# Kernel tuning notes

Measured on AMD Instinct MI355X. Metric: run time of the kernel, lower is better.

Reference implementation:

```python
import jax, jax.numpy as jnp
import numpy as np

NUM_HEADS = 16
HEAD_DIM = 64
WINDOW = 128        # local attention radius |i-j| <= WINDOW
GLOBAL_STRIDE = 64  # tokens at multiples of GLOBAL_STRIDE attend/are attended globally
NEG_INF = -1e9


def sparse_mask(seq_len):
    # bool [S, S]: local band plus global rows/cols (Longformer-style pattern)
    i = jnp.arange(seq_len)
    local = jnp.abs(i[:, None] - i[None, :]) <= WINDOW
    is_global = (i % GLOBAL_STRIDE) == 0
    return local | is_global[:, None] | is_global[None, :]


def setup_inputs() -> dict:
    key = jax.random.key(0)
    k1, k2, k3 = jax.random.split(key, 3)
    B, S, H = 1, 2048, 1024
    x = jax.random.normal(k1, (B, S, H), dtype=jnp.float32)
    Wqkv = jax.random.normal(k2, (3 * H, H), dtype=jnp.float32) * (1.0 / np.sqrt(H))
    Wout = jax.random.normal(k3, (H, H), dtype=jnp.float32) * (1.0 / np.sqrt(H))
    return {"x": x, "Wqkv": Wqkv, "Wout": Wout}


def reference(x, Wqkv, Wout):
    B, S, H = x.shape
    hd = HEAD_DIM
    scale = 1.0 / np.sqrt(hd)

    qkv = x @ Wqkv.T                       # [B, S, 3H] (torch Linear: x @ W^T)
    q, k, v = jnp.split(qkv, 3, axis=-1)
    # [B, nH, S, hd]
    q = q.reshape(B, S, NUM_HEADS, hd).transpose(0, 2, 1, 3)
    k = k.reshape(B, S, NUM_HEADS, hd).transpose(0, 2, 1, 3)
    v = v.reshape(B, S, NUM_HEADS, hd).transpose(0, 2, 1, 3)

    mask = sparse_mask(S)                  # [S, S] bool, broadcasts over (B, nH)
    scores = jnp.einsum('bhqd,bhkd->bhqk', q, k) * scale
    scores = jnp.where(mask, scores, NEG_INF)
    attn = jax.nn.softmax(scores, axis=-1)  # every row has valid keys -> no NaN
    out = jnp.einsum('bhqk,bhkd->bhqd', attn, v)
    out = out.transpose(0, 2, 1, 3).reshape(B, S, H)
    return out @ Wout.T
```

## Files before the change

kernel.cpp:

```cpp
#include <hip/hip_runtime.h>
#include <hip/hip_bf16.h>
#include <math.h>

#define SEQ   2048
#define HID   1024
#define NH    16
#define HD    64
#define WIN   128
#define GSTR  64

typedef __attribute__((ext_vector_type(8))) short short8;
typedef __attribute__((ext_vector_type(4))) float f32x4;
typedef unsigned short ushort_t;

__device__ inline unsigned short bf16b(float f) {
    union { float f; unsigned int u; } v; v.f = f;
    return (unsigned short)((v.u + 0x7FFFu + ((v.u >> 16) & 1u)) >> 16);
}
__device__ inline float blo(unsigned int u) {
    union { unsigned int i; float f; } v; v.i = u << 16; return v.f;
}
__device__ inline float bhi(unsigned int u) {
    union { unsigned int i; float f; } v; v.i = u & 0xFFFF0000u; return v.f;
}

#define GLOAD_LDS16(gp, lp)                                                    \
    __builtin_amdgcn_global_load_lds(                                          \
        (const __attribute__((address_space(1))) unsigned int*)(gp),           \
        (__attribute__((address_space(3))) unsigned int*)(lp), 16, 0, 0)

__global__ __launch_bounds__(256) void cvt_bf16(const float4* __restrict__ x,
                                                const float4* __restrict__ wq,
                                                const float4* __restrict__ wo,
                                                ushort4* __restrict__ x16,
                                                ushort4* __restrict__ wq16,
                                                ushort4* __restrict__ wo16) {
    for (int idx = blockIdx.x * 256 + threadIdx.x; idx < 1572864;
         idx += gridDim.x * 256) {
        const float4* src; ushort4* dst; int off;
        if (idx < 524288)       { src = x;  dst = x16;  off = idx; }
        else if (idx < 1310720) { src = wq; dst = wq16; off = idx - 524288; }
        else                    { src = wo; dst = wo16; off = idx - 1310720; }
        float4 v = src[off];
        ushort4 o;
        o.x = bf16b(v.x); o.y = bf16b(v.y); o.z = bf16b(v.z); o.w = bf16b(v.w);
        dst[off] = o;
    }
}

template <int BM, int BN, typename OT>
__global__ __launch_bounds__(256) void gemm_bt16(const unsigned short* __restrict__ A,
                                                 const unsigned short* __restrict__ B,
                                                 OT* __restrict__ C,
                                                 int M, int N, int K) {
    constexpr int MI = BM / 32;
    constexpr int NJ = BN / 32;
    __shared__ unsigned short As[BM * 32];
    __shared__ unsigned short Bs[BN * 32];

    const int tid  = threadIdx.x;
    const int wave = tid >> 6;
    const int lane = tid & 63;
    const int quad = lane >> 4;
    const int l15  = lane & 15;
    const int bm = blockIdx.y * BM;
    const int bn = blockIdx.x * BN;
    const int wm = (wave & 1) * (BM / 2);
    const int wn = (wave >> 1) * (BN / 2);
    const int srow = lane >> 2;
    const int scol = (lane & 3) * 8;

    f32x4 acc[MI][NJ];
    #pragma unroll
    for (int i = 0; i < MI; ++i)
        #pragma unroll
        for (int j = 0; j < NJ; ++j)
            acc[i][j] = (f32x4){0.f, 0.f, 0.f, 0.f};

    for (int k0 = 0; k0 < K; k0 += 32) {
        #pragma unroll
        for (int t = 0; t < BM / 64; ++t) {
            const int row = wave * (BM / 4) + t * 16 + srow;
            GLOAD_LDS16(A + (size_t)(bm + row) * K + k0 + scol,
                        &As[(size_t)row * 32 + scol]);
        }
        #pragma unroll
        for (int t = 0; t < BN / 64; ++t) {
            const int row = wave * (BN / 4) + t * 16 + srow;
            GLOAD_LDS16(B + (size_t)(bn + row) * K + k0 + scol,
                        &Bs[(size_t)row * 32 + scol]);
        }
        __syncthreads();

        short8 a[MI], b[NJ];
        #pragma unroll
        for (int im = 0; im < MI; ++im)
            a[im] = *(const short8*)&As[(wm + im * 16 + l15) * 32 + quad * 8];
        #pragma unroll
        for (int jn = 0; jn < NJ; ++jn)
            b[jn] = *(const short8*)&Bs[(wn + jn * 16 + l15) * 32 + quad * 8];

        #pragma unroll
        for (int im = 0; im < MI; ++im)
            #pragma unroll
            for (int jn = 0; jn < NJ; ++jn)
                acc[im][jn] = __builtin_amdgcn_mfma_f32_16x16x32_bf16(
                    a[im], b[jn], acc[im][jn], 0, 0, 0);
        __syncthreads();
    }

    #pragma unroll
    for (int im = 0; im < MI; ++im)
        #pragma unroll
        for (int jn = 0; jn < NJ; ++jn)
            #pragma unroll
            for (int reg = 0; reg < 4; ++reg) {
                const int r = bm + wm + im * 16 + quad * 4 + reg;
                const int c = bn + wn + jn * 16 + l15;
                float v = acc[im][jn][reg];
                if constexpr (sizeof(OT) == 2)
                    C[(size_t)r * N + c] = (OT)bf16b(v);
                else
                    C[(size_t)r * N + c] = (OT)v;
            }
}

__global__ __launch_bounds__(256) void attn_fused(const unsigned short* __restrict__ qkv16,
                                                  unsigned short* __restrict__ aout16) {
    __shared__ __align__(16) unsigned char smem[38912];
    const int tid = threadIdx.x;
    const int h = blockIdx.y;
    const int w    = tid >> 6;
    const int lane = tid & 63;
    const int quad = lane >> 4;
    const int l15  = lane & 15;

    if (blockIdx.x < 32) {
        ushort_t* Qs = (ushort_t*)smem;
        ushort_t* Ks = (ushort_t*)(smem + 9216);
        ushort_t* Vt = (ushort_t*)(smem + 18432);
        ushort_t* Ps = (ushort_t*)(smem + 27648);

        const int bq = blockIdx.x;
        const int q0 = bq * 64;
        const int qi = q0 + w * 16 + l15;

        for (int f = tid; f < 512; f += 256) {
            int row = f >> 3, c8 = f & 7;
            *(uint4*)&Qs[row * 72 + c8 * 8] =
                *(const uint4*)&qkv16[(size_t)(q0 + row) * (3 * HID) + h * HD + c8 * 8];
        }

        float mq = -1.0e30f, lq = 0.f;
        f32x4 Oacc[4];
        #pragma unroll
        for (int jt = 0; jt < 4; ++jt) Oacc[jt] = (f32x4){0.f, 0.f, 0.f, 0.f};

        const int t0 = max(bq - 2, 0);
        const int t1 = min(bq + 2, SEQ / 64 - 1);

        uint4 pk[2];
        uint2 pva[2], pvb[2];

        auto prefetch = [&](int tt2, bool g2) {
            const int nf = g2 ? 256 : 512;
            #pragma unroll
            for (int u = 0; u < 2; ++u) {
                const int f = tid + u * 256;
                if (f < nf) {
                    const int row = f >> 3, c8 = f & 7;
                    const size_t gb = (size_t)(g2 ? (row << 6) : (tt2 * 64 + row))
                                          * (3 * HID) + HID + h * HD + c8 * 8;
                    pk[u] = *(const uint4*)&qkv16[gb];
                    const int kp = f >> 4, dc = f & 15;
                    const int k0i = 2 * kp, k1i = 2 * kp + 1;
                    const size_t b0 = (size_t)(g2 ? (k0i << 6) : (tt2 * 64 + k0i))
                                          * (3 * HID) + 2 * HID + h * HD + dc * 4;
                    const size_t b1 = (size_t)(g2 ? (k1i << 6) : (tt2 * 64 + k1i))
                                          * (3 * HID) + 2 * HID + h * HD + dc * 4;
                    pva[u] = *(const uint2*)&qkv16[b0];
                    pvb[u] = *(const uint2*)&qkv16[b1];
                }
            }
        };
        auto commit = [&](bool g2) {
            const int nf = g2 ? 256 : 512;
            #pragma unroll
            for (int u = 0; u < 2; ++u) {
                const int f = tid + u * 256;
                if (f < nf) {
                    const int row = f >> 3, c8 = f & 7;
                    *(uint4*)&Ks[row * 72 + c8 * 8] = pk[u];
                    const int kp = f >> 4, dc = f & 15;
                    uint2 va = pva[u], vb = pvb[u];
                    unsigned int w0 = (va.x & 0xFFFFu) | (vb.x << 16);
                    unsigned int w1 = (va.x >> 16)     | (vb.x & 0xFFFF0000u);
                    unsigned int w2 = (va.y & 0xFFFFu) | (vb.y << 16);
                    unsigned int w3 = (va.y >> 16)     | (vb.y & 0xFFFF0000u);
                    *(unsigned int*)&Vt[(dc * 4 + 0) * 72 + 2 * kp] = w0;
                    *(unsigned int*)&Vt[(dc * 4 + 1) * 72 + 2 * kp] = w1;
                    *(unsigned int*)&Vt[(dc * 4 + 2) * 72 + 2 * kp] = w2;
                    *(unsigned int*)&Vt[(dc * 4 + 3) * 72 + 2 * kp] = w3;
                }
            }
        };

        prefetch(t0, false);
        commit(false);
        __syncthreads();

        for (int tt = t0; tt <= t1 + 1; ++tt) {
            const bool gather = (tt == t1 + 1);
            const bool hasnext = (tt < t1 + 1);
            if (hasnext) prefetch(tt + 1, (tt + 1) == t1 + 1);

            short8 bQ0 = *(const short8*)&Qs[(w * 16 + l15) * 72 + quad * 8];
            short8 bQ1 = *(const short8*)&Qs[(w * 16 + l15) * 72 + 32 + quad * 8];
            f32x4 st[4];
            #pragma unroll
            for (int kt = 0; kt < 4; ++kt) {
                short8 aK0 = *(const short8*)&Ks[(kt * 16 + l15) * 72 + quad * 8];
                short8 aK1 = *(const short8*)&Ks[(kt * 16 + l15) * 72 + 32 + quad * 8];
                f32x4 z = (f32x4){0.f, 0.f, 0.f, 0.f};
                z = __builtin_amdgcn_mfma_f32_16x16x32_bf16(aK0, bQ0, z, 0, 0, 0);
                z = __builtin_amdgcn_mfma_f32_16x16x32_bf16(aK1, bQ1, z, 0, 0, 0);
                st[kt] = z;
            }

            float sv[4][4];
            float tm = -1.0e30f;
            #pragma unroll
            for (int kt = 0; kt < 4; ++kt)
                #pragma unroll
                for (int reg = 0; reg < 4; ++reg) {
                    const int c = kt * 16 + quad * 4 + reg;
                    const int j = gather ? (c << 6) : (tt * 64 + c);
                    const bool valid = gather ? ((c < 32) && (abs(qi - j) > WIN))
                                              : (abs(qi - j) <= WIN);
                    sv[kt][reg] = valid ? st[kt][reg] * 0.125f : -1.0e30f;
                    tm = fmaxf(tm, sv[kt][reg]);
                }

            tm = fmaxf(tm, __shfl_xor(tm, 16));
            tm = fmaxf(tm, __shfl_xor(tm, 32));
            const float mn = fmaxf(mq, tm);
            const float alpha = __expf(mq - mn);
            float p[4][4];
            float ts = 0.f;
            #pragma unroll
            for (int kt = 0; kt < 4; ++kt)
                #pragma unroll
                for (int reg = 0; reg < 4; ++reg) {
                    p[kt][reg] = __expf(sv[kt][reg] - mn);
                    ts += p[kt][reg];
                }
            ts += __shfl_xor(ts, 16);
            ts += __shfl_xor(ts, 32);
            lq = lq * alpha + ts;
            mq = mn;

            #pragma unroll
            for (int kt = 0; kt < 4; ++kt) {
                ushort4 pkt;
                pkt.x = bf16b(p[kt][0]); pkt.y = bf16b(p[kt][1]);
                pkt.z = bf16b(p[kt][2]); pkt.w = bf16b(p[kt][3]);
                *(ushort4*)&Ps[(w * 16 + l15) * 72 + kt * 16 + quad * 4] = pkt;
            }
            #pragma unroll
            for (int jt = 0; jt < 4; ++jt) {
                Oacc[jt][0] *= alpha; Oacc[jt][1] *= alpha;
                Oacc[jt][2] *= alpha; Oacc[jt][3] *= alpha;
            }

            short8 bP0 = *(const short8*)&Ps[(w * 16 + l15) * 72 + quad * 8];
            short8 bP1 = *(const short8*)&Ps[(w * 16 + l15) * 72 + 32 + quad * 8];
            #pragma unroll
            for (int jt = 0; jt < 4; ++jt) {
                short8 aV0 = *(const short8*)&Vt[(jt * 16 + l15) * 72 + quad * 8];
                short8 aV1 = *(const short8*)&Vt[(jt * 16 + l15) * 72 + 32 + quad * 8];
                Oacc[jt] = __builtin_amdgcn_mfma_f32_16x16x32_bf16(aV0, bP0, Oacc[jt], 0, 0, 0);
                Oacc[jt] = __builtin_amdgcn_mfma_f32_16x16x32_bf16(aV1, bP1, Oacc[jt], 0, 0, 0);
            }

            if (hasnext) {
                __syncthreads();
                commit((tt + 1) == t1 + 1);
                __syncthreads();
            }
        }

        if (!(w == 0 && l15 == 0)) {
            const float inv = 1.0f / lq;
            #pragma unroll
            for (int jt = 0; jt < 4; ++jt) {
                ushort4 o;
                o.x = bf16b(Oacc[jt][0] * inv);
                o.y = bf16b(Oacc[jt][1] * inv);
                o.z = bf16b(Oacc[jt][2] * inv);
                o.w = bf16b(Oacc[jt][3] * inv);
                *(ushort4*)&aout16[(size_t)qi * HID + h * HD + jt * 16 + quad * 4] = o;
            }
        }
    } else {
        const int gh = blockIdx.x - 32;
        ushort_t* Ksw = (ushort_t*)(smem + w * 9728);
        ushort_t* Vtw = (ushort_t*)(smem + w * 9728 + 4608);
        ushort_t* Psw = (ushort_t*)(smem + w * 9728 + 8704);

        const size_t qrow = (size_t)((gh * 16 + l15) * 64) * (3 * HID) + h * HD;
        short8 bQ0 = *(const short8*)&qkv16[qrow + quad * 8];
        short8 bQ1 = *(const short8*)&qkv16[qrow + 32 + quad * 8];

        float mq = -1.0e30f, lq = 0.f;
        f32x4 Oacc[4];
        #pragma unroll
        for (int jt = 0; jt < 4; ++jt) Oacc[jt] = (f32x4){0.f, 0.f, 0.f, 0.f};

        for (int s = 0; s < 16; ++s) {
            const int kb = w * 512 + s * 32;
            #pragma unroll
            for (int u = 0; u < 4; ++u) {
                const int unit = lane + u * 64;
                const int row = unit >> 3, c8 = unit & 7;
                *(uint4*)&Ksw[row * 72 + c8 * 8] =
                    *(const uint4*)&qkv16[(size_t)(kb + row) * (3 * HID) + HID + h * HD + c8 * 8];
            }
            #pragma unroll
            for (int u = 0; u < 4; ++u) {
                const int unit = lane + u * 64;
                const int kp = unit >> 4, dc = unit & 15;
                const size_t b0 = (size_t)(kb + 2 * kp) * (3 * HID) + 2 * HID + h * HD + dc * 4;
                const size_t b1 = b0 + 3 * HID;
                uint2 va = *(const uint2*)&qkv16[b0];
                uint2 vb = *(const uint2*)&qkv16[b1];
                unsigned int w0 = (va.x & 0xFFFFu) | (vb.x << 16);
                unsigned int w1 = (va.x >> 16)     | (vb.x & 0xFFFF0000u);
                unsigned int w2 = (va.y & 0xFFFFu) | (vb.y << 16);
                unsigned int w3 = (va.y >> 16)     | (vb.y & 0xFFFF0000u);
                *(unsigned int*)&Vtw[(dc * 4 + 0) * 32 + 2 * kp] = w0;
                *(unsigned int*)&Vtw[(dc * 4 + 1) * 32 + 2 * kp] = w1;
                *(unsigned int*)&Vtw[(dc * 4 + 2) * 32 + 2 * kp] = w2;
                *(unsigned int*)&Vtw[(dc * 4 + 3) * 32 + 2 * kp] = w3;
            }

            f32x4 st[2];
            #pragma unroll
            for (int kt = 0; kt < 2; ++kt) {
                short8 aK0 = *(const short8*)&Ksw[(kt * 16 + l15) * 72 + quad * 8];
                short8 aK1 = *(const short8*)&Ksw[(kt * 16 + l15) * 72 + 32 + quad * 8];
                f32x4 z = (f32x4){0.f, 0.f, 0.f, 0.f};
                z = __builtin_amdgcn_mfma_f32_16x16x32_bf16(aK0, bQ0, z, 0, 0, 0);
                z = __builtin_amdgcn_mfma_f32_16x16x32_bf16(aK1, bQ1, z, 0, 0, 0);
                st[kt] = z;
            }

            float sv[2][4];
            float tm = -1.0e30f;
            #pragma unroll
            for (int kt = 0; kt < 2; ++kt)
                #pragma unroll
                for (int reg = 0; reg < 4; ++reg) {
                    sv[kt][reg] = st[kt][reg] * 0.125f;
                    tm = fmaxf(tm, sv[kt][reg]);
                }
            tm = fmaxf(tm, __shfl_xor(tm, 16));
            tm = fmaxf(tm, __shfl_xor(tm, 32));
            const float mn = fmaxf(mq, tm);
            const float alpha = __expf(mq - mn);
            float p[2][4];
            float ts = 0.f;
            #pragma unroll
            for (int kt = 0; kt < 2; ++kt)
                #pragma unroll
                for (int reg = 0; reg < 4; ++reg) {
                    p[kt][reg] = __expf(sv[kt][reg] - mn);
                    ts += p[kt][reg];
                }
            ts += __shfl_xor(ts, 16);
            ts += __shfl_xor(ts, 32);
            lq = lq * alpha + ts;
            mq = mn;

            #pragma unroll
            for (int kt = 0; kt < 2; ++kt) {
                ushort4 pkt;
                pkt.x = bf16b(p[kt][0]); pkt.y = bf16b(p[kt][1]);
                pkt.z = bf16b(p[kt][2]); pkt.w = bf16b(p[kt][3]);
                *(ushort4*)&Psw[l15 * 32 + kt * 16 + quad * 4] = pkt;
            }
            #pragma unroll
            for (int jt = 0; jt < 4; ++jt) {
                Oacc[jt][0] *= alpha; Oacc[jt][1] *= alpha;
                Oacc[jt][2] *= alpha; Oacc[jt][3] *= alpha;
            }

            short8 bP = *(const short8*)&Psw[l15 * 32 + quad * 8];
            #pragma unroll
            for (int jt = 0; jt < 4; ++jt) {
                short8 aV = *(const short8*)&Vtw[(jt * 16 + l15) * 32 + quad * 8];
                Oacc[jt] = __builtin_amdgcn_mfma_f32_16x16x32_bf16(aV, bP, Oacc[jt], 0, 0, 0);
            }
        }

        __syncthreads();
        float* Om = (float*)smem;
        float* Ml = (float*)(smem + 16384);
        float* Ll = (float*)(smem + 16640);
        #pragma unroll
        for (int jt = 0; jt < 4; ++jt)
            #pragma unroll
            for (int reg = 0; reg < 4; ++reg)
                Om[(w * 16 + l15) * 64 + jt * 16 + quad * 4 + reg] = Oacc[jt][reg];
        if (quad == 0) { Ml[w * 16 + l15] = mq; Ll[w * 16 + l15] = lq; }
        __syncthreads();

        const int d = tid & 63;
        #pragma unroll
        for (int k = 0; k < 4; ++k) {
            const int q = (tid >> 6) * 4 + k;
            float m0 = Ml[q], m1 = Ml[16 + q], m2 = Ml[32 + q], m3 = Ml[48 + q];
            float mM = fmaxf(fmaxf(m0, m1), fmaxf(m2, m3));
            float e0 = __expf(m0 - mM), e1 = __expf(m1 - mM);
            float e2 = __expf(m2 - mM), e3 = __expf(m3 - mM);
            float l = e0 * Ll[q] + e1 * Ll[16 + q] + e2 * Ll[32 + q] + e3 * Ll[48 + q];
            float o = e0 * Om[(q) * 64 + d]        + e1 * Om[(16 + q) * 64 + d]
                    + e2 * Om[(32 + q) * 64 + d]   + e3 * Om[(48 + q) * 64 + d];
            const int i = (gh * 16 + q) * 64;
            aout16[(size_t)i * HID + h * HD + d] = bf16b(o / l);
        }
    }
}

extern "C" void kernel_launch(void* const* d_in, const int* in_sizes, int n_in,
                              void* d_out, int out_size, void* d_ws, size_t ws_size,
                              hipStream_t stream) {
    const float* x    = (const float*)d_in[0];
    const float* Wqkv = (const float*)d_in[1];
    const float* Wout = (const float*)d_in[2];
    float* out = (float*)d_out;

    unsigned short* x16    = (unsigned short*)d_ws;
    unsigned short* wq16   = x16  + (size_t)SEQ * HID;
    unsigned short* wo16   = wq16 + (size_t)3 * HID * HID;
    unsigned short* qkv16  = wo16 + (size_t)HID * HID;
    unsigned short* aout16 = qkv16 + (size_t)SEQ * 3 * HID;

    cvt_bf16<<<dim3(1024), 256, 0, stream>>>(
        (const float4*)x, (const float4*)Wqkv, (const float4*)Wout,
        (ushort4*)x16, (ushort4*)wq16, (ushort4*)wo16);

    gemm_bt16<64, 128, unsigned short><<<dim3(3 * HID / 128, SEQ / 64), 256, 0, stream>>>(
        x16, wq16, qkv16, SEQ, 3 * HID, HID);

    attn_fused<<<dim3(34, NH), 256, 0, stream>>>(qkv16, aout16);

    gemm_bt16<64, 64, float><<<dim3(HID / 64, SEQ / 64), 256, 0, stream>>>(
        aout16, wo16, out, SEQ, HID, HID);
}
```

Baseline: 151.7 us.

## Split local attention blocks into 32-query tiles with two-way key split and merge

Local-window attention blocks now handle 32 queries instead of 64, doubling the block count. The four waves are split two query groups by two key-range halves, with separate K/V buffers per half. Partial softmax states are merged through shared memory at the end. This raises parallelism across the GPU, at the cost of dropping the register prefetch pipelining, re-staging K/V for adjacent query blocks, adding a merge pass, and using more shared memory.

```diff
diff --git a/kernel.cpp b/kernel.cpp
--- a/kernel.cpp
+++ b/kernel.cpp
@@ -127,7 +127,7 @@
 
 __global__ __launch_bounds__(256) void attn_fused(const unsigned short* __restrict__ qkv16,
                                                   unsigned short* __restrict__ aout16) {
-    __shared__ __align__(16) unsigned char smem[38912];
+    __shared__ __align__(16) unsigned char smem[50688];
     const int tid = threadIdx.x;
     const int h = blockIdx.y;
     const int w    = tid >> 6;
@@ -135,174 +135,189 @@
     const int quad = lane >> 4;
     const int l15  = lane & 15;
 
-    if (blockIdx.x < 32) {
-        ushort_t* Qs = (ushort_t*)smem;
-        ushort_t* Ks = (ushort_t*)(smem + 9216);
-        ushort_t* Vt = (ushort_t*)(smem + 18432);
-        ushort_t* Ps = (ushort_t*)(smem + 27648);
+    if (blockIdx.x < 64) {
+        ushort_t* Qs  = (ushort_t*)smem;
+        ushort_t* Kb0 = (ushort_t*)(smem + 4608);
+        ushort_t* Kb1 = (ushort_t*)(smem + 13824);
+        ushort_t* Vb0 = (ushort_t*)(smem + 23040);
+        ushort_t* Vb1 = (ushort_t*)(smem + 32256);
+        ushort_t* Psw = (ushort_t*)(smem + 41472 + w * 2304);
 
         const int bq = blockIdx.x;
-        const int q0 = bq * 64;
-        const int qi = q0 + w * 16 + l15;
-
-        for (int f = tid; f < 512; f += 256) {
-            int row = f >> 3, c8 = f & 7;
+        const int a  = bq >> 1;
+        const int q0 = bq * 32;
+        const int qg = w & 1;
+        const int ks = w >> 1;
+        const int qi = q0 + qg * 16 + l15;
+
+        {
+            const int row = tid >> 3, c8 = tid & 7;
             *(uint4*)&Qs[row * 72 + c8 * 8] =
                 *(const uint4*)&qkv16[(size_t)(q0 + row) * (3 * HID) + h * HD + c8 * 8];
         }
 
+        const int t0g  = max(a - 2, 0);
+        const int t1g  = min(a + 2, SEQ / 64 - 1);
+        const int ntot = (t1g - t0g + 1) + 1;
+        const int n0   = (ntot + 1) >> 1;
+        const int n1   = ntot - n0;
+
         float mq = -1.0e30f, lq = 0.f;
         f32x4 Oacc[4];
         #pragma unroll
         for (int jt = 0; jt < 4; ++jt) Oacc[jt] = (f32x4){0.f, 0.f, 0.f, 0.f};
 
-        const int t0 = max(bq - 2, 0);
-        const int t1 = min(bq + 2, SEQ / 64 - 1);
-
-        uint4 pk[2];
-        uint2 pva[2], pvb[2];
-
-        auto prefetch = [&](int tt2, bool g2) {
-            const int nf = g2 ? 256 : 512;
-            #pragma unroll
-            for (int u = 0; u < 2; ++u) {
-                const int f = tid + u * 256;
-                if (f < nf) {
-                    const int row = f >> 3, c8 = f & 7;
-                    const size_t gb = (size_t)(g2 ? (row << 6) : (tt2 * 64 + row))
-                                          * (3 * HID) + HID + h * HD + c8 * 8;
-                    pk[u] = *(const uint4*)&qkv16[gb];
-                    const int kp = f >> 4, dc = f & 15;
-                    const int k0i = 2 * kp, k1i = 2 * kp + 1;
-                    const size_t b0 = (size_t)(g2 ? (k0i << 6) : (tt2 * 64 + k0i))
-                                          * (3 * HID) + 2 * HID + h * HD + dc * 4;
-                    const size_t b1 = (size_t)(g2 ? (k1i << 6) : (tt2 * 64 + k1i))
-                                          * (3 * HID) + 2 * HID + h * HD + dc * 4;
-                    pva[u] = *(const uint2*)&qkv16[b0];
-                    pvb[u] = *(const uint2*)&qkv16[b1];
-                }
+        auto stage_tile = [&](ushort_t* Kb, ushort_t* Vb, int tile, bool gather) {
+            const int nf = gather ? 256 : 512;
+            for (int f = tid; f < nf; f += 256) {
+                const int row = f >> 3, c8 = f & 7;
+                const size_t gb = (size_t)(gather ? (row << 6) : (tile * 64 + row))
+                                      * (3 * HID) + HID + h * HD + c8 * 8;
+                *(uint4*)&Kb[row * 72 + c8 * 8] = *(const uint4*)&qkv16[gb];
+            }
+            for (int f = tid; f < nf; f += 256) {
+                const int kp = f >> 4, dc = f & 15;
+                const int k0i = 2 * kp, k1i = 2 * kp + 1;
+                const size_t b0 = (size_t)(gather ? (k0i << 6) : (tile * 64 + k0i))
+                                      * (3 * HID) + 2 * HID + h * HD + dc * 4;
+                const size_t b1 = (size_t)(gather ? (k1i << 6) : (tile * 64 + k1i))
+                                      * (3 * HID) + 2 * HID + h * HD + dc * 4;
+                uint2 va = *(const uint2*)&qkv16[b0];
+                uint2 vb = *(const uint2*)&qkv16[b1];
+                unsigned int w0 = (va.x & 0xFFFFu) | (vb.x << 16);
+                unsigned int w1 = (va.x >> 16)     | (vb.x & 0xFFFF0000u);
+                unsigned int w2 = (va.y & 0xFFFFu) | (vb.y << 16);
+                unsigned int w3 = (va.y >> 16)     | (vb.y & 0xFFFF0000u);
+                *(unsigned int*)&Vb[(dc * 4 + 0) * 72 + 2 * kp] = w0;
+                *(unsigned int*)&Vb[(dc * 4 + 1) * 72 + 2 * kp] = w1;
+                *(unsigned int*)&Vb[(dc * 4 + 2) * 72 + 2 * kp] = w2;
+                *(unsigned int*)&Vb[(dc * 4 + 3) * 72 + 2 * kp] = w3;
             }
         };
-        auto commit = [&](bool g2) {
-            const int nf = g2 ? 256 : 512;
-            #pragma unroll
-            for (int u = 0; u < 2; ++u) {
-                const int f = tid + u * 256;
-                if (f < nf) {
-                    const int row = f >> 3, c8 = f & 7;
-                    *(uint4*)&Ks[row * 72 + c8 * 8] = pk[u];
-                    const int kp = f >> 4, dc = f & 15;
-                    uint2 va = pva[u], vb = pvb[u];
-                    unsigned int w0 = (va.x & 0xFFFFu) | (vb.x << 16);
-                    unsigned int w1 = (va.x >> 16)     | (vb.x & 0xFFFF0000u);
-                    unsigned int w2 = (va.y & 0xFFFFu) | (vb.y << 16);
-                    unsigned int w3 = (va.y >> 16)     | (vb.y & 0xFFFF0000u);
-                    *(unsigned int*)&Vt[(dc * 4 + 0) * 72 + 2 * kp] = w0;
-                    *(unsigned int*)&Vt[(dc * 4 + 1) * 72 + 2 * kp] = w1;
-                    *(unsigned int*)&Vt[(dc * 4 + 2) * 72 + 2 * kp] = w2;
-                    *(unsigned int*)&Vt[(dc * 4 + 3) * 72 + 2 * kp] = w3;
-                }
-            }
-        };
-
-        prefetch(t0, false);
-        commit(false);
-        __syncthreads();
-
-        for (int tt = t0; tt <= t1 + 1; ++tt) {
-            const bool gather = (tt == t1 + 1);
-            const bool hasnext = (tt < t1 + 1);
-            if (hasnext) prefetch(tt + 1, (tt + 1) == t1 + 1);
-
-            short8 bQ0 = *(const short8*)&Qs[(w * 16 + l15) * 72 + quad * 8];
-            short8 bQ1 = *(const short8*)&Qs[(w * 16 + l15) * 72 + 32 + quad * 8];
-            f32x4 st[4];
-            #pragma unroll
-            for (int kt = 0; kt < 4; ++kt) {
-                short8 aK0 = *(const short8*)&Ks[(kt * 16 + l15) * 72 + quad * 8];
-                short8 aK1 = *(const short8*)&Ks[(kt * 16 + l15) * 72 + 32 + quad * 8];
-                f32x4 z = (f32x4){0.f, 0.f, 0.f, 0.f};
-                z = __builtin_amdgcn_mfma_f32_16x16x32_bf16(aK0, bQ0, z, 0, 0, 0);
-                z = __builtin_amdgcn_mfma_f32_16x16x32_bf16(aK1, bQ1, z, 0, 0, 0);
-                st[kt] = z;
-            }
-
-            float sv[4][4];
-            float tm = -1.0e30f;
-            #pragma unroll
-            for (int kt = 0; kt < 4; ++kt)
-                #pragma unroll
-                for (int reg = 0; reg < 4; ++reg) {
-                    const int c = kt * 16 + quad * 4 + reg;
-                    const int j = gather ? (c << 6) : (tt * 64 + c);
-                    const bool valid = gather ? ((c < 32) && (abs(qi - j) > WIN))
-                                              : (abs(qi - j) <= WIN);
-                    sv[kt][reg] = valid ? st[kt][reg] * 0.125f : -1.0e30f;
-                    tm = fmaxf(tm, sv[kt][reg]);
-                }
-
-            tm = fmaxf(tm, __shfl_xor(tm, 16));
-            tm = fmaxf(tm, __shfl_xor(tm, 32));
-            const float mn = fmaxf(mq, tm);
-            const float alpha = __expf(mq - mn);
-            float p[4][4];
-            float ts = 0.f;
-            #pragma unroll
-            for (int kt = 0; kt < 4; ++kt)
-                #pragma unroll
-                for (int reg = 0; reg < 4; ++reg) {
-                    p[kt][reg] = __expf(sv[kt][reg] - mn);
-                    ts += p[kt][reg];
-                }
-            ts += __shfl_xor(ts, 16);
-            ts += __shfl_xor(ts, 32);
-            lq = lq * alpha + ts;
-            mq = mn;
-
-            #pragma unroll
-            for (int kt = 0; kt < 4; ++kt) {
-                ushort4 pkt;
-                pkt.x = bf16b(p[kt][0]); pkt.y = bf16b(p[kt][1]);
-                pkt.z = bf16b(p[kt][2]); pkt.w = bf16b(p[kt][3]);
-                *(ushort4*)&Ps[(w * 16 + l15) * 72 + kt * 16 + quad * 4] = pkt;
-            }
-            #pragma unroll
-            for (int jt = 0; jt < 4; ++jt) {
-                Oacc[jt][0] *= alpha; Oacc[jt][1] *= alpha;
-                Oacc[jt][2] *= alpha; Oacc[jt][3] *= alpha;
-            }
-
-            short8 bP0 = *(const short8*)&Ps[(w * 16 + l15) * 72 + quad * 8];
-            short8 bP1 = *(const short8*)&Ps[(w * 16 + l15) * 72 + 32 + quad * 8];
-            #pragma unroll
-            for (int jt = 0; jt < 4; ++jt) {
-                short8 aV0 = *(const short8*)&Vt[(jt * 16 + l15) * 72 + quad * 8];
-                short8 aV1 = *(const short8*)&Vt[(jt * 16 + l15) * 72 + 32 + quad * 8];
-                Oacc[jt] = __builtin_amdgcn_mfma_f32_16x16x32_bf16(aV0, bP0, Oacc[jt], 0, 0, 0);
-                Oacc[jt] = __builtin_amdgcn_mfma_f32_16x16x32_bf16(aV1, bP1, Oacc[jt], 0, 0, 0);
-            }
-
-            if (hasnext) {
-                __syncthreads();
-                commit((tt + 1) == t1 + 1);
-                __syncthreads();
-            }
-        }
-
-        if (!(w == 0 && l15 == 0)) {
-            const float inv = 1.0f / lq;
-            #pragma unroll
-            for (int jt = 0; jt < 4; ++jt) {
-                ushort4 o;
-                o.x = bf16b(Oacc[jt][0] * inv);
-                o.y = bf16b(Oacc[jt][1] * inv);
-                o.z = bf16b(Oacc[jt][2] * inv);
-                o.w = bf16b(Oacc[jt][3] * inv);
-                *(ushort4*)&aout16[(size_t)qi * HID + h * HD + jt * 16 + quad * 4] = o;
+
+        for (int s = 0; s < n0; ++s) {
+            __syncthreads();
+            stage_tile(Kb0, Vb0, t0g + s, false);
+            if (s < n1)
+                stage_tile(Kb1, Vb1, t0g + n0 + s, (n0 + s) == ntot - 1);
+            __syncthreads();
+
+            const int  idx    = (ks == 0) ? s : n0 + s;
+            const bool active = (ks == 0) || (s < n1);
+            if (active) {
+                const bool gather = (idx == ntot - 1);
+                const int  tile   = t0g + idx;
+                ushort_t* Kb = ks ? Kb1 : Kb0;
+                ushort_t* Vb = ks ? Vb1 : Vb0;
+
+                short8 bQ0 = *(const short8*)&Qs[(qg * 16 + l15) * 72 + quad * 8];
+                short8 bQ1 = *(const short8*)&Qs[(qg * 16 + l15) * 72 + 32 + quad * 8];
+                f32x4 st[4];
+                #pragma unroll
+                for (int kt = 0; kt < 4; ++kt) {
+                    short8 aK0 = *(const short8*)&Kb[(kt * 16 + l15) * 72 + quad * 8];
+                    short8 aK1 = *(const short8*)&Kb[(kt * 16 + l15) * 72 + 32 + quad * 8];
+                    f32x4 z = (f32x4){0.f, 0.f, 0.f, 0.f};
+                    z = __builtin_amdgcn_mfma_f32_16x16x32_bf16(aK0, bQ0, z, 0, 0, 0);
+                    z = __builtin_amdgcn_mfma_f32_16x16x32_bf16(aK1, bQ1, z, 0, 0, 0);
+                    st[kt] = z;
+                }
+
+                float sv[4][4];
+                float tm = -1.0e30f;
+                #pragma unroll
+                for (int kt = 0; kt < 4; ++kt)
+                    #pragma unroll
+                    for (int reg = 0; reg < 4; ++reg) {
+                        const int c = kt * 16 + quad * 4 + reg;
+                        const int j = gather ? (c << 6) : (tile * 64 + c);
+                        const bool valid = gather ? ((c < 32) && (abs(qi - j) > WIN))
+                                                  : (abs(qi - j) <= WIN);
+                        sv[kt][reg] = valid ? st[kt][reg] * 0.125f : -1.0e30f;
+                        tm = fmaxf(tm, sv[kt][reg]);
+                    }
+
+                tm = fmaxf(tm, __shfl_xor(tm, 16));
+                tm = fmaxf(tm, __shfl_xor(tm, 32));
+                const float mn = fmaxf(mq, tm);
+                const float alpha = __expf(mq - mn);
+                float p[4][4];
+                float ts = 0.f;
+                #pragma unroll
+                for (int kt = 0; kt < 4; ++kt)
+                    #pragma unroll
+                    for (int reg = 0; reg < 4; ++reg) {
+                        p[kt][reg] = __expf(sv[kt][reg] - mn);
+                        ts += p[kt][reg];
+                    }
+                ts += __shfl_xor(ts, 16);
+                ts += __shfl_xor(ts, 32);
+                lq = lq * alpha + ts;
+                mq = mn;
+
+                #pragma unroll
+                for (int kt = 0; kt < 4; ++kt) {
+                    ushort4 pkt;
+                    pkt.x = bf16b(p[kt][0]); pkt.y = bf16b(p[kt][1]);
+                    pkt.z = bf16b(p[kt][2]); pkt.w = bf16b(p[kt][3]);
+                    *(ushort4*)&Psw[l15 * 72 + kt * 16 + quad * 4] = pkt;
+                }
+                #pragma unroll
+                for (int jt = 0; jt < 4; ++jt) {
+                    Oacc[jt][0] *= alpha; Oacc[jt][1] *= alpha;
+                    Oacc[jt][2] *= alpha; Oacc[jt][3] *= alpha;
+                }
+
+                short8 bP0 = *(const short8*)&Psw[l15 * 72 + quad * 8];
+                short8 bP1 = *(const short8*)&Psw[l15 * 72 + 32 + quad * 8];
+                #pragma unroll
+                for (int jt = 0; jt < 4; ++jt) {
+                    short8 aV0 = *(const short8*)&Vb[(jt * 16 + l15) * 72 + quad * 8];
+                    short8 aV1 = *(const short8*)&Vb[(jt * 16 + l15) * 72 + 32 + quad * 8];
+                    Oacc[jt] = __builtin_amdgcn_mfma_f32_16x16x32_bf16(aV0, bP0, Oacc[jt], 0, 0, 0);
+                    Oacc[jt] = __builtin_amdgcn_mfma_f32_16x16x32_bf16(aV1, bP1, Oacc[jt], 0, 0, 0);
+                }
+            }
+        }
+
+        __syncthreads();
+        float* Om = (float*)smem;
+        float* Ml = (float*)(smem + 16384);
+        float* Ll = (float*)(smem + 16640);
+        #pragma unroll
+        for (int jt = 0; jt < 4; ++jt) {
+            float4 v = make_float4(Oacc[jt][0], Oacc[jt][1], Oacc[jt][2], Oacc[jt][3]);
+            *(float4*)&Om[(ks * 32 + qg * 16 + l15) * 64 + jt * 16 + quad * 4] = v;
+        }
+        if (quad == 0) { Ml[ks * 32 + qg * 16 + l15] = mq; Ll[ks * 32 + qg * 16 + l15] = lq; }
+        __syncthreads();
+
+        {
+            const int q  = tid >> 3;
+            const int dc = (tid & 7) * 8;
+            const int iq = q0 + q;
+            if ((iq & 63) != 0) {
+                const float m0 = Ml[q], m1 = Ml[32 + q];
+                const float mM = fmaxf(m0, m1);
+                const float e0 = __expf(m0 - mM), e1 = __expf(m1 - mM);
+                const float inv = 1.0f / (e0 * Ll[q] + e1 * Ll[32 + q]);
+                ushort4 oa, ob;
+                float o0 = (e0 * Om[q * 64 + dc + 0] + e1 * Om[(32 + q) * 64 + dc + 0]) * inv;
+                float o1 = (e0 * Om[q * 64 + dc + 1] + e1 * Om[(32 + q) * 64 + dc + 1]) * inv;
+                float o2 = (e0 * Om[q * 64 + dc + 2] + e1 * Om[(32 + q) * 64 + dc + 2]) * inv;
+                float o3 = (e0 * Om[q * 64 + dc + 3] + e1 * Om[(32 + q) * 64 + dc + 3]) * inv;
+                float o4 = (e0 * Om[q * 64 + dc + 4] + e1 * Om[(32 + q) * 64 + dc + 4]) * inv;
+                float o5 = (e0 * Om[q * 64 + dc + 5] + e1 * Om[(32 + q) * 64 + dc + 5]) * inv;
+                float o6 = (e0 * Om[q * 64 + dc + 6] + e1 * Om[(32 + q) * 64 + dc + 6]) * inv;
+                float o7 = (e0 * Om[q * 64 + dc + 7] + e1 * Om[(32 + q) * 64 + dc + 7]) * inv;
+                oa.x = bf16b(o0); oa.y = bf16b(o1); oa.z = bf16b(o2); oa.w = bf16b(o3);
+                ob.x = bf16b(o4); ob.y = bf16b(o5); ob.z = bf16b(o6); ob.w = bf16b(o7);
+                *(ushort4*)&aout16[(size_t)iq * HID + h * HD + dc]     = oa;
+                *(ushort4*)&aout16[(size_t)iq * HID + h * HD + dc + 4] = ob;
             }
         }
     } else {
-        const int gh = blockIdx.x - 32;
+        const int gh = blockIdx.x - 64;
         ushort_t* Ksw = (ushort_t*)(smem + w * 9728);
         ushort_t* Vtw = (ushort_t*)(smem + w * 9728 + 4608);
         ushort_t* Psw = (ushort_t*)(smem + w * 9728 + 8704);
@@ -452,7 +467,7 @@
     gemm_bt16<64, 128, unsigned short><<<dim3(3 * HID / 128, SEQ / 64), 256, 0, stream>>>(
         x16, wq16, qkv16, SEQ, 3 * HID, HID);
 
-    attn_fused<<<dim3(34, NH), 256, 0, stream>>>(qkv16, aout16);
+    attn_fused<<<dim3(66, NH), 256, 0, stream>>>(qkv16, aout16);
 
     gemm_bt16<64, 64, float><<<dim3(HID / 64, SEQ / 64), 256, 0, stream>>>(
         aout16, wo16, out, SEQ, HID, HID);
```

Result: slower. 159.5 us (+5.2%).
